# Kernel tuning notes

Measured on AMD Instinct MI355X. Metric: run time of the kernel, lower is better.

## Reference

```python
import jax, jax.numpy as jnp
import numpy as np

B, N, D_IN, D_OUT = 4, 2048, 1024, 1024


def setup_inputs() -> dict:
    key = jax.random.key(0)
    kx, kq, kk, kv = jax.random.split(key, 4)
    x = jax.random.normal(kx, (B, N, D_IN), dtype=jnp.float32)
    # torch Linear(d_in, d_out, bias=False): y = x @ W.T, W ~ U(-1/sqrt(d_in), 1/sqrt(d_in)).
    # Store as [d_in, d_out] so y = x @ W.
    bound = 1.0 / np.sqrt(D_IN)
    Wq = jax.random.uniform(kq, (D_IN, D_OUT), jnp.float32, -bound, bound)
    Wk = jax.random.uniform(kk, (D_IN, D_OUT), jnp.float32, -bound, bound)
    Wv = jax.random.uniform(kv, (D_IN, D_OUT), jnp.float32, -bound, bound)
    return {"x": x, "Wq": Wq, "Wk": Wk, "Wv": Wv}


def reference(x, Wq, Wk, Wv):
    # x: [B, N, d_in]
    q = jnp.einsum("bnd,de->bne", x, Wq)  # [B, N, d_out]
    k = jnp.einsum("bnd,de->bne", x, Wk)
    v = jnp.einsum("bnd,de->bne", x, Wv)
    n = x.shape[1]
    scores = jnp.einsum("bqe,bke->bqk", q, k)  # [B, N, N]
    causal = jnp.triu(jnp.ones((n, n), dtype=bool), k=1)  # True above diagonal -> masked
    scores = jnp.where(causal, -jnp.inf, scores)
    scale = 1.0 / jnp.sqrt(jnp.asarray(k.shape[-1], dtype=scores.dtype))
    weights = jax.nn.softmax(scores * scale, axis=-1)
    # dropout with drop_rate=0.0 is identity
    return jnp.einsum("bqk,bke->bqe", weights, v)  # [B, N, d_out]
```

## Files before the change

kernel.cpp:

```cpp
#include <hip/hip_runtime.h>

typedef float  f4v  __attribute__((ext_vector_type(4)));
typedef short  s8v  __attribute__((ext_vector_type(8)));

__device__ __forceinline__ ushort f2b(float f) {
    union { float f; unsigned int u; } v; v.f = f;
    unsigned int u = v.u;
    u += 0x7fffu + ((u >> 16) & 1u);
    return (ushort)(u >> 16);
}
__device__ __forceinline__ float b2f(ushort u) {
    union { unsigned int u; float f; } v; v.u = ((unsigned int)u) << 16;
    return v.f;
}

__device__ __forceinline__ void async16(const ushort* g, ushort* ldsp) {
    __builtin_amdgcn_global_load_lds(
        (const __attribute__((address_space(1))) unsigned int*)g,
        (__attribute__((address_space(3))) unsigned int*)ldsp, 16, 0, 0);
}

__global__ __launch_bounds__(256) void cast_f32_bf16(const float* __restrict__ in,
                                                     ushort* __restrict__ out,
                                                     float* __restrict__ l, int n4) {
    int i = blockIdx.x * 256 + threadIdx.x;
    if (i < 8192) l[i] = 0.f;
    if (i < n4) {
        float4 f = ((const float4*)in)[i];
        ushort4 o;
        o.x = f2b(f.x); o.y = f2b(f.y); o.z = f2b(f.z); o.w = f2b(f.w);
        ((ushort4*)out)[i] = o;
    }
}

__global__ __launch_bounds__(256) void transpose_cast(const float* __restrict__ w0,
                                                      const float* __restrict__ w1,
                                                      const float* __restrict__ w2,
                                                      ushort* __restrict__ out) {
    __shared__ float tile[32][33];
    const float* W = (blockIdx.z == 0) ? w0 : (blockIdx.z == 1 ? w1 : w2);
    ushort* O = out + (size_t)blockIdx.z * (1024u * 1024u);
    int x0 = blockIdx.x * 32, y0 = blockIdx.y * 32;
    int tx = threadIdx.x, ty = threadIdx.y;
    for (int i = 0; i < 4; i++)
        tile[ty + i * 8][tx] = W[(size_t)(y0 + ty + i * 8) * 1024 + x0 + tx];
    __syncthreads();
    for (int i = 0; i < 4; i++)
        O[(size_t)(x0 + ty + i * 8) * 1024 + y0 + tx] = f2b(tile[tx][ty + i * 8]);
}


#define RD_A4(buf_)                                                                   \
    _Pragma("unroll") for (int mi = 0; mi < 4; mi++)                                  \
    _Pragma("unroll") for (int s = 0; s < 2; s++)                                     \
        af[mi][s] = *(const s8v*)&(buf_)[(wm + mi * 16 + l16) * 64 +                  \
                                         (((s * 4 + quad) ^ (l16 & 7)) * 8)];

#define RD_B2(buf_, NI0_)                                                             \
    _Pragma("unroll") for (int j = 0; j < 2; j++)                                     \
    _Pragma("unroll") for (int s = 0; s < 2; s++)                                     \
        bf[j][s] = *(const s8v*)&(buf_)[(wn + ((NI0_) + j) * 16 + l16) * 64 +         \
                                        (((s * 4 + quad) ^ (l16 & 7)) * 8)];

#define MFMA16(NI0_)                                                                  \
    _Pragma("unroll") for (int mi = 0; mi < 4; mi++)                                  \
    _Pragma("unroll") for (int j = 0; j < 2; j++)                                     \
    _Pragma("unroll") for (int s = 0; s < 2; s++)                                     \
        acc[mi][(NI0_) + j] = __builtin_amdgcn_mfma_f32_16x16x32_bf16(                \
            af[mi][s], bf[j][s], acc[mi][(NI0_) + j], 0, 0, 0);

__global__ __launch_bounds__(512, 2) void gemm_qkv(const ushort* __restrict__ A,
                                                   const ushort* __restrict__ Wt,
                                                   ushort* __restrict__ q,
                                                   ushort* __restrict__ k,
                                                   ushort* __restrict__ vt) {
    constexpr int K = 1024;
    extern __shared__ ushort lds[];

    const int L = blockIdx.x;
    const int xcd = L & 7, idx = L >> 3;
    const int ci = xcd >> 1, cj = xcd & 1;
    const int mo = idx >> 3, no = idx & 7;
    const int m0 = (ci * 8 + mo) * 256;
    const int n0 = (cj * 8 + no) * 192;

    const int tid = threadIdx.x;
    const int w = tid >> 6, lane = tid & 63, quad = lane >> 4, l16 = lane & 15;
    const int wm = (w >> 1) * 64, wn = (w & 1) * 96;

    ushort* a0 = lds;
    ushort* a1 = lds + 16384;
    ushort* a2 = lds + 32768;
    ushort* b0 = lds + 49152;
    ushort* b1 = lds + 61440;

    const int lr = lane >> 3;
    const int lc8 = (lane & 7) ^ lr;
    const ushort* Ab = A  + (size_t)(m0 + w * 8 + lr) * K + lc8 * 8;
    const ushort* Bb = Wt + (size_t)(n0 + w * 8 + lr) * K + lc8 * 8;
    const int dW = w * 512;

#define ISSUE_A(buf_, kk_, a_) async16(Ab + (size_t)(a_) * 64 * K + (kk_), (buf_) + (a_) * 4096 + dW)
#define ISSUE_B(buf_, kk_, c_) async16(Bb + (size_t)(c_) * 64 * K + (kk_), (buf_) + (c_) * 4096 + dW)

    f4v acc[4][6];
    #pragma unroll
    for (int mi = 0; mi < 4; mi++)
        #pragma unroll
        for (int ni = 0; ni < 6; ni++) acc[mi][ni] = 0;

    #pragma unroll
    for (int a = 0; a < 4; a++) ISSUE_A(a0, 0, a);
    #pragma unroll
    for (int c = 0; c < 3; c++) ISSUE_B(b0, 0, c);
    #pragma unroll
    for (int a = 0; a < 4; a++) ISSUE_A(a1, 64, a);
    asm volatile("s_waitcnt vmcnt(4)" ::: "memory");
    asm volatile("s_barrier" ::: "memory");

    for (int t = 0; t < 16; ++t) {
        const int kB = (t + 1) * 64;
        const int kA = (t + 2) * 64;
        s8v af[4][2], bf[2][2];

        RD_A4(a0)
        RD_B2(b0, 0)
        if (t < 15) {
            ISSUE_B(b1, kB, 0);
            ISSUE_B(b1, kB, 1);
            ISSUE_B(b1, kB, 2);
        }
        asm volatile("s_barrier" ::: "memory");
        __builtin_amdgcn_s_setprio(1);
        MFMA16(0)
        __builtin_amdgcn_s_setprio(0);
        asm volatile("s_barrier" ::: "memory");

        RD_B2(b0, 2)
        if (t < 14) {
            ISSUE_A(a2, kA, 0);
            ISSUE_A(a2, kA, 1);
        }
        asm volatile("s_barrier" ::: "memory");
        __builtin_amdgcn_s_setprio(1);
        MFMA16(2)
        __builtin_amdgcn_s_setprio(0);
        asm volatile("s_barrier" ::: "memory");

        RD_B2(b0, 4)
        if (t < 14) {
            ISSUE_A(a2, kA, 2);
            ISSUE_A(a2, kA, 3);
        }
        asm volatile("s_barrier" ::: "memory");
        __builtin_amdgcn_s_setprio(1);
        MFMA16(4)
        __builtin_amdgcn_s_setprio(0);

        if (t < 14)       asm volatile("s_waitcnt vmcnt(4)" ::: "memory");
        else if (t == 14) asm volatile("s_waitcnt vmcnt(0)" ::: "memory");
        asm volatile("s_barrier" ::: "memory");

        ushort* ta = a0; a0 = a1; a1 = a2; a2 = ta;
        ushort* tb = b0; b0 = b1; b1 = tb;
    }

    #pragma unroll
    for (int mi = 0; mi < 4; mi++)
        #pragma unroll
        for (int ni = 0; ni < 6; ni++) {
            int row = m0 + wm + mi * 16 + quad * 4;
            int col = n0 + wn + ni * 16 + l16;
            int z = col >> 10, cz = col & 1023;
            f4v v = acc[mi][ni];
            if (z < 2) {
                ushort* C = (z == 0) ? q : k;
                #pragma unroll
                for (int rr = 0; rr < 4; rr++)
                    C[(size_t)(row + rr) * 1024 + cz] = f2b(v[rr]);
            } else {
                int b = row >> 11, tok = row & 2047;
                ushort4 pk;
                pk.x = f2b(v[0]); pk.y = f2b(v[1]); pk.z = f2b(v[2]); pk.w = f2b(v[3]);
                *(ushort4*)&vt[(size_t)b * (1024u * 2048u) + (size_t)cz * 2048 + tok] = pk;
            }
        }
#undef ISSUE_A
#undef ISSUE_B
}

__global__ __launch_bounds__(512, 2) void sgemm_qk(const ushort* __restrict__ Q,
                                                   const ushort* __restrict__ Km,
                                                   ushort* __restrict__ E,
                                                   float* __restrict__ l) {
    constexpr int K = 1024;
    extern __shared__ ushort lds[];

    const int L = blockIdx.x;
    const int xcd = L & 7, i = L >> 3;
    const int t = (xcd < 4) ? (xcd * 26 + i) : (104 + (xcd - 4) * 25 + i);
    const int b = t / 51;
    int tt = t - b * 51;
    int mt = 0;
    for (;; mt++) {
        int c = (4 * (mt + 1) + 2) / 3;
        if (tt < c) break;
        tt -= c;
    }
    const int nt = tt;
    const int m0 = mt * 256, n0 = nt * 192;
    const ushort* A  = Q  + (size_t)b * 2048 * 1024;
    const ushort* Bt = Km + (size_t)b * 2048 * 1024;
    ushort* Cb = E + (size_t)b * 2048 * 2048;
    float* lb = l + (size_t)b * 2048;

    const int tid = threadIdx.x;
    const int w = tid >> 6, lane = tid & 63, quad = lane >> 4, l16 = lane & 15;
    const int wm = (w >> 1) * 64, wn = (w & 1) * 96;

    ushort* a0 = lds;
    ushort* a1 = lds + 16384;
    ushort* a2 = lds + 32768;
    ushort* b0 = lds + 49152;
    ushort* b1 = lds + 61440;

    const int lr = lane >> 3;
    const int lc8 = (lane & 7) ^ lr;
    const ushort* Ab = A  + (size_t)(m0 + w * 8 + lr) * K + lc8 * 8;
    const ushort* Bb = Bt + (size_t)(n0 + w * 8 + lr) * K + lc8 * 8;
    const int dW = w * 512;

#define ISSUE_A(buf_, kk_, a_) async16(Ab + (size_t)(a_) * 64 * K + (kk_), (buf_) + (a_) * 4096 + dW)
#define ISSUE_B(buf_, kk_, c_) async16(Bb + (size_t)(c_) * 64 * K + (kk_), (buf_) + (c_) * 4096 + dW)

    f4v acc[4][6];
    #pragma unroll
    for (int mi = 0; mi < 4; mi++)
        #pragma unroll
        for (int ni = 0; ni < 6; ni++) acc[mi][ni] = 0;

    #pragma unroll
    for (int a = 0; a < 4; a++) ISSUE_A(a0, 0, a);
    #pragma unroll
    for (int c = 0; c < 3; c++) ISSUE_B(b0, 0, c);
    #pragma unroll
    for (int a = 0; a < 4; a++) ISSUE_A(a1, 64, a);
    asm volatile("s_waitcnt vmcnt(4)" ::: "memory");
    asm volatile("s_barrier" ::: "memory");

    for (int tk = 0; tk < 16; ++tk) {
        const int kB = (tk + 1) * 64;
        const int kA = (tk + 2) * 64;
        s8v af[4][2], bf[2][2];

        RD_A4(a0)
        RD_B2(b0, 0)
        if (tk < 15) {
            ISSUE_B(b1, kB, 0);
            ISSUE_B(b1, kB, 1);
            ISSUE_B(b1, kB, 2);
        }
        asm volatile("s_barrier" ::: "memory");
        __builtin_amdgcn_s_setprio(1);
        MFMA16(0)
        __builtin_amdgcn_s_setprio(0);
        asm volatile("s_barrier" ::: "memory");

        RD_B2(b0, 2)
        if (tk < 14) {
            ISSUE_A(a2, kA, 0);
            ISSUE_A(a2, kA, 1);
        }
        asm volatile("s_barrier" ::: "memory");
        __builtin_amdgcn_s_setprio(1);
        MFMA16(2)
        __builtin_amdgcn_s_setprio(0);
        asm volatile("s_barrier" ::: "memory");

        RD_B2(b0, 4)
        if (tk < 14) {
            ISSUE_A(a2, kA, 2);
            ISSUE_A(a2, kA, 3);
        }
        asm volatile("s_barrier" ::: "memory");
        __builtin_amdgcn_s_setprio(1);
        MFMA16(4)
        __builtin_amdgcn_s_setprio(0);

        if (tk < 14)       asm volatile("s_waitcnt vmcnt(4)" ::: "memory");
        else if (tk == 14) asm volatile("s_waitcnt vmcnt(0)" ::: "memory");
        asm volatile("s_barrier" ::: "memory");

        ushort* ta = a0; a0 = a1; a1 = a2; a2 = ta;
        ushort* tb = b0; b0 = b1; b1 = tb;
    }

    #pragma unroll
    for (int mi = 0; mi < 4; mi++) {
        float rs[4] = {0.f, 0.f, 0.f, 0.f};
        #pragma unroll
        for (int ni = 0; ni < 6; ni++) {
            const int colbase = n0 + wn + ni * 16;
            if (colbase >= 2048) continue;
            const int col = colbase + l16;
            f4v v = acc[mi][ni];
            #pragma unroll
            for (int rr = 0; rr < 4; rr++) {
                const int row = m0 + wm + mi * 16 + quad * 4 + rr;
                float e = (col <= row) ? __expf(v[rr] * 0.03125f) : 0.f;
                ushort eb = f2b(e);
                Cb[(size_t)row * 2048 + col] = eb;
                rs[rr] += b2f(eb);
            }
        }
        #pragma unroll
        for (int rr = 0; rr < 4; rr++) {
            float s = rs[rr];
            s += __shfl_xor(s, 1);
            s += __shfl_xor(s, 2);
            s += __shfl_xor(s, 4);
            s += __shfl_xor(s, 8);
            if (l16 == 0)
                atomicAdd(&lb[m0 + wm + mi * 16 + quad * 4 + rr], s);
        }
    }
#undef ISSUE_A
#undef ISSUE_B
}

__global__ __launch_bounds__(512, 2) void gemm_pv(const ushort* __restrict__ Em,
                                                  const ushort* __restrict__ Vt,
                                                  const float* __restrict__ l,
                                                  float* __restrict__ Out) {
    extern __shared__ ushort lds[];
    const int L = blockIdx.x;
    int p, mt;
    if (L < 256) { p = L;       mt = 15 - (p >> 5); }
    else         { p = L - 256; mt = (p >> 5); }
    const int inner = p & 31;
    const int b = inner >> 3;
    const int nt = inner & 7;
    const int m0 = mt * 128, n0 = nt * 128;
    const int NT = 2 * (mt + 1);
    const ushort* A  = Em + (size_t)b * 2048 * 2048;
    const ushort* Bt = Vt + (size_t)b * 1024 * 2048;
    const float* lb = l + (size_t)b * 2048;
    float* C = Out + (size_t)b * 2048 * 1024;

    const int tid = threadIdx.x;
    const int w = tid >> 6, lane = tid & 63, quad = lane >> 4, l16 = lane & 15;
    const int wm = (w >> 2) * 64, wn = (w & 3) * 32;

    ushort* a0 = lds;
    ushort* a1 = lds + 8192;
    ushort* a2 = lds + 16384;
    ushort* b0 = lds + 24576;
    ushort* b1 = lds + 32768;

    const int lr = lane >> 3;
    const int lc8 = (lane & 7) ^ lr;
    const ushort* Ab = A  + (size_t)(m0 + w * 8 + lr) * 2048 + lc8 * 8;
    const ushort* Bb = Bt + (size_t)(n0 + w * 8 + lr) * 2048 + lc8 * 8;
    const int dW = w * 512;

#define ISSUE_A(buf_, kk_, a_) async16(Ab + (size_t)(a_) * 64 * 2048 + (kk_), (buf_) + (a_) * 4096 + dW)
#define ISSUE_B(buf_, kk_, c_) async16(Bb + (size_t)(c_) * 64 * 2048 + (kk_), (buf_) + (c_) * 4096 + dW)

    f4v acc[4][2];
    #pragma unroll
    for (int mi = 0; mi < 4; mi++)
        #pragma unroll
        for (int ni = 0; ni < 2; ni++) acc[mi][ni] = 0;

    #pragma unroll
    for (int a = 0; a < 2; a++) ISSUE_A(a0, 0, a);
    #pragma unroll
    for (int c = 0; c < 2; c++) ISSUE_B(b0, 0, c);
    #pragma unroll
    for (int a = 0; a < 2; a++) ISSUE_A(a1, 64, a);
    asm volatile("s_waitcnt vmcnt(2)" ::: "memory");
    asm volatile("s_barrier" ::: "memory");

    for (int tk = 0; tk < NT; ++tk) {
        const int kB = (tk + 1) * 64;
        const int kA = (tk + 2) * 64;
        s8v af[4][2], bf[2][2];

        RD_A4(a0)
        RD_B2(b0, 0)
        if (tk < NT - 1) {
            ISSUE_B(b1, kB, 0);
            ISSUE_B(b1, kB, 1);
        }
        if (tk < NT - 2) {
            ISSUE_A(a2, kA, 0);
            ISSUE_A(a2, kA, 1);
        }
        asm volatile("s_barrier" ::: "memory");
        __builtin_amdgcn_s_setprio(1);
        MFMA16(0)
        __builtin_amdgcn_s_setprio(0);

        if (tk < NT - 2)       asm volatile("s_waitcnt vmcnt(2)" ::: "memory");
        else if (tk == NT - 2) asm volatile("s_waitcnt vmcnt(0)" ::: "memory");
        asm volatile("s_barrier" ::: "memory");

        ushort* ta = a0; a0 = a1; a1 = a2; a2 = ta;
        ushort* tb = b0; b0 = b1; b1 = tb;
    }

    #pragma unroll
    for (int mi = 0; mi < 4; mi++) {
        const int row = m0 + wm + mi * 16 + quad * 4;
        float inv[4];
        #pragma unroll
        for (int rr = 0; rr < 4; rr++) inv[rr] = 1.f / lb[row + rr];
        #pragma unroll
        for (int ni = 0; ni < 2; ni++) {
            const int col = n0 + wn + ni * 16 + l16;
            f4v v = acc[mi][ni];
            #pragma unroll
            for (int rr = 0; rr < 4; rr++)
                C[(size_t)(row + rr) * 1024 + col] = v[rr] * inv[rr];
        }
    }
#undef ISSUE_A
#undef ISSUE_B
}

extern "C" void kernel_launch(void* const* d_in, const int* in_sizes, int n_in,
                              void* d_out, int out_size, void* d_ws, size_t ws_size,
                              hipStream_t stream) {
    const float* x  = (const float*)d_in[0];
    const float* Wq = (const float*)d_in[1];
    const float* Wk = (const float*)d_in[2];
    const float* Wv = (const float*)d_in[3];
    float* out = (float*)d_out;

    static bool init = false;
    if (!init) {
        hipFuncSetAttribute(reinterpret_cast<const void*>(gemm_qkv),
                            hipFuncAttributeMaxDynamicSharedMemorySize, 147456);
        hipFuncSetAttribute(reinterpret_cast<const void*>(sgemm_qk),
                            hipFuncAttributeMaxDynamicSharedMemorySize, 147456);
        hipFuncSetAttribute(reinterpret_cast<const void*>(gemm_pv),
                            hipFuncAttributeMaxDynamicSharedMemorySize, 81920);
        init = true;
    }

    char* ws = (char*)d_ws;
    const size_t MiB = 1u << 20;
    ushort* xb = (ushort*)(ws);
    ushort* wt = (ushort*)(ws + 16 * MiB);
    ushort* q  = (ushort*)(ws + 22 * MiB);
    ushort* k  = (ushort*)(ws + 38 * MiB);
    ushort* vt = (ushort*)(ws + 54 * MiB);
    ushort* E  = (ushort*)(ws + 70 * MiB);
    float*  l  = (float*)(ws + 102 * MiB);

    cast_f32_bf16<<<(8192 * 1024 / 4) / 256, 256, 0, stream>>>(x, xb, l, 8192 * 1024 / 4);
    transpose_cast<<<dim3(32, 32, 3), dim3(32, 8), 0, stream>>>(Wq, Wk, Wv, wt);

    gemm_qkv<<<512, 512, 147456, stream>>>(xb, wt, q, k, vt);
    sgemm_qk<<<204, 512, 147456, stream>>>(q, k, E, l);
    gemm_pv<<<512, 512, 81920, stream>>>(E, vt, l, out);
}
```

Before: 208.3 us.

## Pair complementary causal tiles per block in PV GEMM and fuse prep kernels

The PV GEMM now launches half as many blocks. Each block processes two row tiles, mt and 15-mt, in sequence, so every block gets an equal amount of causal work. The separate cast and weight-transpose kernels are merged into a single prep launch, which saves one kernel launch. The risk is reduced parallelism: 256 blocks may leave occupancy slots unused compared with 512 blocks scheduled dynamically.

Result: slower. 214.6 us (+3.0%).

```diff
diff --git a/kernel.cpp b/kernel.cpp
--- a/kernel.cpp
+++ b/kernel.cpp
@@ -20,28 +20,31 @@
         (__attribute__((address_space(3))) unsigned int*)ldsp, 16, 0, 0);
 }
 
-__global__ __launch_bounds__(256) void cast_f32_bf16(const float* __restrict__ in,
-                                                     ushort* __restrict__ out,
-                                                     float* __restrict__ l, int n4) {
-    int i = blockIdx.x * 256 + threadIdx.x;
-    if (i < 8192) l[i] = 0.f;
-    if (i < n4) {
+__global__ __launch_bounds__(256) void prep(const float* __restrict__ in,
+                                            ushort* __restrict__ out,
+                                            float* __restrict__ l,
+                                            const float* __restrict__ w0,
+                                            const float* __restrict__ w1,
+                                            const float* __restrict__ w2,
+                                            ushort* __restrict__ wt) {
+    const int L = blockIdx.x, tid = threadIdx.x;
+    if (L < 8192) {
+        int i = L * 256 + tid;
+        if (i < 8192) l[i] = 0.f;
         float4 f = ((const float4*)in)[i];
         ushort4 o;
         o.x = f2b(f.x); o.y = f2b(f.y); o.z = f2b(f.z); o.w = f2b(f.w);
         ((ushort4*)out)[i] = o;
-    }
-}
-
-__global__ __launch_bounds__(256) void transpose_cast(const float* __restrict__ w0,
-                                                      const float* __restrict__ w1,
-                                                      const float* __restrict__ w2,
-                                                      ushort* __restrict__ out) {
+        return;
+    }
     __shared__ float tile[32][33];
-    const float* W = (blockIdx.z == 0) ? w0 : (blockIdx.z == 1 ? w1 : w2);
-    ushort* O = out + (size_t)blockIdx.z * (1024u * 1024u);
-    int x0 = blockIdx.x * 32, y0 = blockIdx.y * 32;
-    int tx = threadIdx.x, ty = threadIdx.y;
+    const int T = L - 8192;
+    const int z = T >> 10, rem = T & 1023;
+    const int bx = rem & 31, by = rem >> 5;
+    const float* W = (z == 0) ? w0 : (z == 1 ? w1 : w2);
+    ushort* O = wt + (size_t)z * (1024u * 1024u);
+    int x0 = bx * 32, y0 = by * 32;
+    int tx = tid & 31, ty = tid >> 5;
     for (int i = 0; i < 4; i++)
         tile[ty + i * 8][tx] = W[(size_t)(y0 + ty + i * 8) * 1024 + x0 + tx];
     __syncthreads();
@@ -334,14 +337,12 @@
                                                   float* __restrict__ Out) {
     extern __shared__ ushort lds[];
     const int L = blockIdx.x;
-    int p, mt;
-    if (L < 256) { p = L;       mt = 15 - (p >> 5); }
-    else         { p = L - 256; mt = (p >> 5); }
+    const int p = (L & 7) * 32 + (L >> 3);
+    const int pair = p >> 5;
     const int inner = p & 31;
     const int b = inner >> 3;
     const int nt = inner & 7;
-    const int m0 = mt * 128, n0 = nt * 128;
-    const int NT = 2 * (mt + 1);
+    const int n0 = nt * 128;
     const ushort* A  = Em + (size_t)b * 2048 * 2048;
     const ushort* Bt = Vt + (size_t)b * 1024 * 2048;
     const float* lb = l + (size_t)b * 2048;
@@ -351,77 +352,85 @@
     const int w = tid >> 6, lane = tid & 63, quad = lane >> 4, l16 = lane & 15;
     const int wm = (w >> 2) * 64, wn = (w & 3) * 32;
 
-    ushort* a0 = lds;
-    ushort* a1 = lds + 8192;
-    ushort* a2 = lds + 16384;
-    ushort* b0 = lds + 24576;
-    ushort* b1 = lds + 32768;
-
     const int lr = lane >> 3;
     const int lc8 = (lane & 7) ^ lr;
-    const ushort* Ab = A  + (size_t)(m0 + w * 8 + lr) * 2048 + lc8 * 8;
-    const ushort* Bb = Bt + (size_t)(n0 + w * 8 + lr) * 2048 + lc8 * 8;
     const int dW = w * 512;
 
 #define ISSUE_A(buf_, kk_, a_) async16(Ab + (size_t)(a_) * 64 * 2048 + (kk_), (buf_) + (a_) * 4096 + dW)
 #define ISSUE_B(buf_, kk_, c_) async16(Bb + (size_t)(c_) * 64 * 2048 + (kk_), (buf_) + (c_) * 4096 + dW)
 
-    f4v acc[4][2];
-    #pragma unroll
-    for (int mi = 0; mi < 4; mi++)
-        #pragma unroll
-        for (int ni = 0; ni < 2; ni++) acc[mi][ni] = 0;
-
-    #pragma unroll
-    for (int a = 0; a < 2; a++) ISSUE_A(a0, 0, a);
-    #pragma unroll
-    for (int c = 0; c < 2; c++) ISSUE_B(b0, 0, c);
-    #pragma unroll
-    for (int a = 0; a < 2; a++) ISSUE_A(a1, 64, a);
-    asm volatile("s_waitcnt vmcnt(2)" ::: "memory");
-    asm volatile("s_barrier" ::: "memory");
-
-    for (int tk = 0; tk < NT; ++tk) {
-        const int kB = (tk + 1) * 64;
-        const int kA = (tk + 2) * 64;
-        s8v af[4][2], bf[2][2];
-
-        RD_A4(a0)
-        RD_B2(b0, 0)
-        if (tk < NT - 1) {
-            ISSUE_B(b1, kB, 0);
-            ISSUE_B(b1, kB, 1);
-        }
-        if (tk < NT - 2) {
-            ISSUE_A(a2, kA, 0);
-            ISSUE_A(a2, kA, 1);
-        }
-        asm volatile("s_barrier" ::: "memory");
-        __builtin_amdgcn_s_setprio(1);
-        MFMA16(0)
-        __builtin_amdgcn_s_setprio(0);
-
-        if (tk < NT - 2)       asm volatile("s_waitcnt vmcnt(2)" ::: "memory");
-        else if (tk == NT - 2) asm volatile("s_waitcnt vmcnt(0)" ::: "memory");
-        asm volatile("s_barrier" ::: "memory");
-
-        ushort* ta = a0; a0 = a1; a1 = a2; a2 = ta;
-        ushort* tb = b0; b0 = b1; b1 = tb;
-    }
-
-    #pragma unroll
-    for (int mi = 0; mi < 4; mi++) {
-        const int row = m0 + wm + mi * 16 + quad * 4;
-        float inv[4];
-        #pragma unroll
-        for (int rr = 0; rr < 4; rr++) inv[rr] = 1.f / lb[row + rr];
-        #pragma unroll
-        for (int ni = 0; ni < 2; ni++) {
-            const int col = n0 + wn + ni * 16 + l16;
-            f4v v = acc[mi][ni];
+    #pragma unroll
+    for (int half = 0; half < 2; ++half) {
+        const int mt = half ? (15 - pair) : pair;
+        const int m0 = mt * 128;
+        const int NT = 2 * (mt + 1);
+
+        ushort* a0 = lds;
+        ushort* a1 = lds + 8192;
+        ushort* a2 = lds + 16384;
+        ushort* b0 = lds + 24576;
+        ushort* b1 = lds + 32768;
+
+        const ushort* Ab = A  + (size_t)(m0 + w * 8 + lr) * 2048 + lc8 * 8;
+        const ushort* Bb = Bt + (size_t)(n0 + w * 8 + lr) * 2048 + lc8 * 8;
+
+        f4v acc[4][2];
+        #pragma unroll
+        for (int mi = 0; mi < 4; mi++)
             #pragma unroll
-            for (int rr = 0; rr < 4; rr++)
-                C[(size_t)(row + rr) * 1024 + col] = v[rr] * inv[rr];
+            for (int ni = 0; ni < 2; ni++) acc[mi][ni] = 0;
+
+        #pragma unroll
+        for (int a = 0; a < 2; a++) ISSUE_A(a0, 0, a);
+        #pragma unroll
+        for (int c = 0; c < 2; c++) ISSUE_B(b0, 0, c);
+        #pragma unroll
+        for (int a = 0; a < 2; a++) ISSUE_A(a1, 64, a);
+        asm volatile("s_waitcnt vmcnt(2)" ::: "memory");
+        asm volatile("s_barrier" ::: "memory");
+
+        for (int tk = 0; tk < NT; ++tk) {
+            const int kB = (tk + 1) * 64;
+            const int kA = (tk + 2) * 64;
+            s8v af[4][2], bf[2][2];
+
+            RD_A4(a0)
+            RD_B2(b0, 0)
+            if (tk < NT - 1) {
+                ISSUE_B(b1, kB, 0);
+                ISSUE_B(b1, kB, 1);
+            }
+            if (tk < NT - 2) {
+                ISSUE_A(a2, kA, 0);
+                ISSUE_A(a2, kA, 1);
+            }
+            asm volatile("s_barrier" ::: "memory");
+            __builtin_amdgcn_s_setprio(1);
+            MFMA16(0)
+            __builtin_amdgcn_s_setprio(0);
+
+            if (tk < NT - 2)       asm volatile("s_waitcnt vmcnt(2)" ::: "memory");
+            else if (tk == NT - 2) asm volatile("s_waitcnt vmcnt(0)" ::: "memory");
+            asm volatile("s_barrier" ::: "memory");
+
+            ushort* ta = a0; a0 = a1; a1 = a2; a2 = ta;
+            ushort* tb = b0; b0 = b1; b1 = tb;
+        }
+
+        #pragma unroll
+        for (int mi = 0; mi < 4; mi++) {
+            const int row = m0 + wm + mi * 16 + quad * 4;
+            float inv[4];
+            #pragma unroll
+            for (int rr = 0; rr < 4; rr++) inv[rr] = 1.f / lb[row + rr];
+            #pragma unroll
+            for (int ni = 0; ni < 2; ni++) {
+                const int col = n0 + wn + ni * 16 + l16;
+                f4v v = acc[mi][ni];
+                #pragma unroll
+                for (int rr = 0; rr < 4; rr++)
+                    C[(size_t)(row + rr) * 1024 + col] = v[rr] * inv[rr];
+            }
         }
     }
 #undef ISSUE_A
@@ -458,10 +467,9 @@
     ushort* E  = (ushort*)(ws + 70 * MiB);
     float*  l  = (float*)(ws + 102 * MiB);
 
-    cast_f32_bf16<<<(8192 * 1024 / 4) / 256, 256, 0, stream>>>(x, xb, l, 8192 * 1024 / 4);
-    transpose_cast<<<dim3(32, 32, 3), dim3(32, 8), 0, stream>>>(Wq, Wk, Wv, wt);
+    prep<<<8192 + 3072, 256, 0, stream>>>(x, xb, l, Wq, Wk, Wv, wt);
 
     gemm_qkv<<<512, 512, 147456, stream>>>(xb, wt, q, k, vt);
     sgemm_qk<<<204, 512, 147456, stream>>>(q, k, E, l);
-    gemm_pv<<<512, 512, 81920, stream>>>(E, vt, l, out);
-}
+    gemm_pv<<<256, 512, 81920, stream>>>(E, vt, l, out);
+}
```
